# Performance work log

Hardware: AMD Instinct MI355X
Metric: run time of the kernel (lower is better)

## Reference

```python
import jax, jax.numpy as jnp
import numpy as np

B, S, E = 2, 4096, 2560
H, HKV, D = 8, 4, 256
WINDOW = 1024
SOFTCAP = 50.0
SCALING = 256.0 ** -0.5  # query_pre_attn_scalar = 256
EPS = 1e-6
MASK_VAL = -2.3819763e38


def rms_norm(x, w):
    # RMSNorm with add_unit_offset=True, computed in float32
    xf = x.astype(jnp.float32)
    out = xf * jax.lax.rsqrt(jnp.mean(xf * xf, axis=-1, keepdims=True) + EPS)
    return (out * (1.0 + w.astype(jnp.float32))).astype(x.dtype)


def apply_rotary_emb(x, cos, sin):
    # x: [B, S, h, D]; cos/sin: [S, D/2]; half-split rotation
    x1, x2 = jnp.split(x, 2, axis=-1)
    c = cos[None, :, None, :]
    s = sin[None, :, None, :]
    return jnp.concatenate([x1 * c - x2 * s, x2 * c + x1 * s], axis=-1)


def setup_inputs() -> dict:
    key = jax.random.key(0)
    ks = jax.random.split(key, 6)
    hidden_states = jax.random.normal(ks[0], (B, S, E), dtype=jnp.float32)
    # RoPE frequencies, theta=10000
    inv_freq = 1.0 / (10000.0 ** (np.arange(0, D, 2, dtype=np.float32) / D))
    t = np.arange(S, dtype=np.float32)
    freqs = np.outer(t, inv_freq)  # [S, D/2]
    freqs_cos = jnp.asarray(np.cos(freqs), dtype=jnp.float32)
    freqs_sin = jnp.asarray(np.sin(freqs), dtype=jnp.float32)
    kv_write_indices = jnp.arange(S, dtype=jnp.int32)
    k_cache = jnp.zeros((B, S, HKV, D), dtype=jnp.float32)
    v_cache = jnp.zeros((B, S, HKV, D), dtype=jnp.float32)
    # causal mask and causal+sliding-window mask (additive)
    i = np.arange(S)[:, None]
    j = np.arange(S)[None, :]
    causal = j <= i
    sliding = causal & ((i - j) < WINDOW)
    mask = jnp.asarray(np.where(causal, 0.0, MASK_VAL), dtype=jnp.float32)
    mask = jnp.broadcast_to(mask[None, None], (B, 1, S, S))
    local_mask = jnp.asarray(np.where(sliding, 0.0, MASK_VAL), dtype=jnp.float32)
    local_mask = jnp.broadcast_to(local_mask[None, None], (B, 1, S, S))
    w_qkv = jax.random.normal(ks[1], ((H + 2 * HKV) * D, E), dtype=jnp.float32) * (E ** -0.5)
    w_o = jax.random.normal(ks[2], (E, H * D), dtype=jnp.float32) * ((H * D) ** -0.5)
    q_norm_w = jnp.zeros((D,), dtype=jnp.float32)
    k_norm_w = jnp.zeros((D,), dtype=jnp.float32)
    return dict(hidden_states=hidden_states, freqs_cos=freqs_cos, freqs_sin=freqs_sin,
                kv_write_indices=kv_write_indices, k_cache=k_cache, v_cache=v_cache,
                mask=mask, local_mask=local_mask, w_qkv=w_qkv, w_o=w_o,
                q_norm_w=q_norm_w, k_norm_w=k_norm_w)


def reference(hidden_states, freqs_cos, freqs_sin, kv_write_indices, k_cache, v_cache,
              mask, local_mask, w_qkv, w_o, q_norm_w, k_norm_w):
    bsz, input_len, _ = hidden_states.shape
    qkv = jnp.einsum('bse,fe->bsf', hidden_states, w_qkv)
    xq, xk, xv = jnp.split(qkv, [H * D, H * D + HKV * D], axis=-1)
    xq = xq.reshape(bsz, input_len, H, D)
    xk = xk.reshape(bsz, input_len, HKV, D)
    xv = xv.reshape(bsz, input_len, HKV, D)
    # QK RMSNorm
    xq = rms_norm(xq, q_norm_w)
    xk = rms_norm(xk, k_norm_w)
    # RoPE
    xq = apply_rotary_emb(xq, freqs_cos, freqs_sin)
    xk = apply_rotary_emb(xk, freqs_cos, freqs_sin)
    # KV cache write
    k_cache = k_cache.at[:, kv_write_indices].set(xk)
    v_cache = v_cache.at[:, kv_write_indices].set(xv)
    kv_len = k_cache.shape[1]
    # GQA expand: [B, T, HKV, D] -> [B, T, H, D]
    nrep = H // HKV
    key = jnp.repeat(k_cache, nrep, axis=2)
    value = jnp.repeat(v_cache, nrep, axis=2)
    q = jnp.transpose(xq, (0, 2, 1, 3)) * SCALING   # [B, H, S, D]
    k = jnp.transpose(key, (0, 2, 1, 3))            # [B, H, T, D]
    v = jnp.transpose(value, (0, 2, 1, 3))
    scores = jnp.einsum('bhqd,bhkd->bhqk', q, k)
    # logit softcapping
    scores = jnp.tanh(scores / SOFTCAP) * SOFTCAP
    # attn_type == LOCAL_SLIDING -> use local (sliding-window) mask
    scores = scores + local_mask
    probs = jax.nn.softmax(scores.astype(jnp.float32), axis=-1).astype(q.dtype)
    out = jnp.einsum('bhqk,bhkd->bhqd', probs, v)
    out = jnp.transpose(out, (0, 2, 1, 3)).reshape(bsz, input_len, H * D)
    return jnp.einsum('bsf,ef->bse', out, w_o)
```

## Files before the change

### kernel.cpp

```cpp
#include <hip/hip_runtime.h>
#include <stdint.h>
#include <stddef.h>

#define B_    2
#define S_    4096
#define E_    2560
#define H_    8
#define HKV_  4
#define D_    256
#define F_    4096
#define HD_   2048
#define WIN_  1024
#define MASKNEG (-3.0e38f)

typedef __bf16 bf16;
typedef bf16  bf16x8 __attribute__((ext_vector_type(8)));
typedef bf16  bf16x4 __attribute__((ext_vector_type(4)));
typedef float f32x4  __attribute__((ext_vector_type(4)));
typedef uint32_t u32;

__device__ __forceinline__ void gl_lds16(const void* g, void* l) {
  __builtin_amdgcn_global_load_lds((const __attribute__((address_space(1))) void*)g,
                                   (__attribute__((address_space(3))) void*)l, 16, 0, 0);
}

__device__ __forceinline__ float softcap50(float x) {
  float t = x * 0.02f;
  t = fminf(fmaxf(t, -15.f), 15.f);
  float e = __expf(2.f * t);
  return 50.f * ((e - 1.f) / (e + 1.f));
}

__device__ __forceinline__ u32 pkbf16(float a, float b) {
  union { bf16 h[2]; u32 u; } cv;
  cv.h[0] = (bf16)a; cv.h[1] = (bf16)b; return cv.u;
}

__global__ __launch_bounds__(256) void to_bf16_plain(const float* __restrict__ src,
                                                     bf16* __restrict__ dst, int n) {
  const int i = (blockIdx.x * 256 + threadIdx.x) * 8;
  if (i >= n) return;
  f32x4 a = *(const f32x4*)(src + i);
  f32x4 b = *(const f32x4*)(src + i + 4);
  bf16x8 o;
#pragma unroll
  for (int j = 0; j < 4; ++j) { o[j] = (bf16)a[j]; o[j + 4] = (bf16)b[j]; }
  *(bf16x8*)(dst + i) = o;
}

__global__ __launch_bounds__(256) void gemm1_bf(const bf16* __restrict__ A,
                                                const bf16* __restrict__ W,
                                                bf16* __restrict__ qo,
                                                bf16* __restrict__ ko,
                                                bf16* __restrict__ vto,
                                                int row_base) {
  __shared__ bf16 As[128 * 32];
  __shared__ bf16 Bs[128 * 32];
  const int tid  = threadIdx.x;
  const int lane = tid & 63;
  const int l16  = lane & 15;
  const int quad = lane >> 4;
  const int wave = tid >> 6;
  const int wm   = wave & 1;
  const int wn   = wave >> 1;

  const int lrow0 = blockIdx.y * 128;
  const int col0  = blockIdx.x * 128;

  const int srow = tid >> 2;
  const int scol = (tid & 3) * 8;

  const bf16* Ab = A + (size_t)lrow0 * E_ + scol;
  const bf16* Bb = W + (size_t)col0 * E_ + scol;

  f32x4 acc[4][4] = {};

  for (int k0 = 0; k0 < E_; k0 += 32) {
    gl_lds16(Ab + (size_t)srow * E_ + k0,        As + tid * 8);
    gl_lds16(Ab + (size_t)(srow + 64) * E_ + k0, As + 2048 + tid * 8);
    gl_lds16(Bb + (size_t)srow * E_ + k0,        Bs + tid * 8);
    gl_lds16(Bb + (size_t)(srow + 64) * E_ + k0, Bs + 2048 + tid * 8);
    __syncthreads();

    bf16x8 af[4], bfr[4];
#pragma unroll
    for (int i = 0; i < 4; ++i)
      af[i] = *(const bf16x8*)&As[(wm * 64 + i * 16 + l16) * 32 + quad * 8];
#pragma unroll
    for (int i = 0; i < 4; ++i)
      bfr[i] = *(const bf16x8*)&Bs[(wn * 64 + i * 16 + l16) * 32 + quad * 8];
#pragma unroll
    for (int i = 0; i < 4; ++i)
#pragma unroll
      for (int j = 0; j < 4; ++j)
        acc[i][j] = __builtin_amdgcn_mfma_f32_16x16x32_bf16(af[i], bfr[j], acc[i][j], 0, 0, 0);
    __syncthreads();
  }

#pragma unroll
  for (int i = 0; i < 4; ++i) {
    const int rbase = row_base + lrow0 + wm * 64 + i * 16 + quad * 4;
#pragma unroll
    for (int j = 0; j < 4; ++j) {
      const int c = col0 + wn * 64 + j * 16 + l16;
      int head = c >> 8;
      const int d = c & 255;
      if (head < 12) {
        bf16* base;
        int nh;
        if (head < 8) { base = qo; nh = H_; }
        else          { base = ko; nh = HKV_; head -= 8; }
#pragma unroll
        for (int rr = 0; rr < 4; ++rr) {
          const int row = rbase + rr;
          const int b = row >> 12, s = row & 4095;
          base[(((size_t)(b * nh + head) * S_) + s) * D_ + d] = (bf16)acc[i][j][rr];
        }
      } else {
        const int kh = head - 12;
        const int b  = rbase >> 12, s0 = rbase & 4095;
        bf16x4 pk;
#pragma unroll
        for (int rr = 0; rr < 4; ++rr) pk[rr] = (bf16)acc[i][j][rr];
        *(bf16x4*)(vto + (((size_t)(b * HKV_ + kh) * D_ + d) * S_ + s0)) = pk;
      }
    }
  }
}

__global__ __launch_bounds__(192) void normrope2(
    bf16* __restrict__ q, bf16* __restrict__ k,
    const float* __restrict__ fcos, const float* __restrict__ fsin,
    const int* __restrict__ widx,
    const float* __restrict__ qnw, const float* __restrict__ knw) {
  const int bx  = blockIdx.x;
  const int b   = bx >> 12;
  const int s   = bx & 4095;
  const int tid = threadIdx.x;
  const int hh  = tid >> 4;
  const int g   = tid & 15;
  const int d0  = g * 16;

  const bool isq = (hh < 8);
  bf16* rowp = isq ? (q + (((size_t)(b * H_ + hh) * S_ + s) * D_ + d0))
                   : (k + (((size_t)(b * HKV_ + (hh - 8)) * S_ + s) * D_ + d0));
  float x[16];
  {
    bf16x8 v0 = *(const bf16x8*)rowp;
    bf16x8 v1 = *(const bf16x8*)(rowp + 8);
#pragma unroll
    for (int i = 0; i < 8; ++i) { x[i] = (float)v0[i]; x[i + 8] = (float)v1[i]; }
  }

  float ssq = 0.f;
#pragma unroll
  for (int i = 0; i < 16; ++i) ssq += x[i] * x[i];
#pragma unroll
  for (int off = 1; off < 16; off <<= 1) ssq += __shfl_xor(ssq, off);
  const float sc = rsqrtf(ssq * (1.0f / 256.0f) + 1e-6f);
  const float* w = isq ? qnw : knw;
#pragma unroll
  for (int i = 0; i < 16; ++i) x[i] = x[i] * sc * (1.0f + w[d0 + i]);

  const int fbase = (g < 8) ? d0 : (d0 - 128);
  const float* cp = fcos + (size_t)s * 128 + fbase;
  const float* sp = fsin + (size_t)s * 128 + fbase;
#pragma unroll
  for (int i = 0; i < 16; ++i) {
    const float c = cp[i], sn = sp[i];
    const float other = __shfl_xor(x[i], 8);
    x[i] = (g < 8) ? (x[i] * c - other * sn)
                   : (x[i] * c + other * sn);
  }
  if (isq) {
#pragma unroll
    for (int i = 0; i < 16; ++i) x[i] *= 0.0625f;
  }

  bf16x8 o0, o1;
#pragma unroll
  for (int i = 0; i < 8; ++i) { o0[i] = (bf16)x[i]; o1[i] = (bf16)x[i + 8]; }

  bf16* dstp = isq ? rowp
                   : (k + (((size_t)(b * HKV_ + (hh - 8)) * S_ + widx[s]) * D_ + d0));
  *(bf16x8*)dstp = o0;
  *(bf16x8*)(dstp + 8) = o1;
}

__global__ __launch_bounds__(256) void attn_mfma(const bf16* __restrict__ Q,
                                                 const bf16* __restrict__ K,
                                                 const bf16* __restrict__ Vt,
                                                 bf16* __restrict__ out) {
  __shared__ bf16 Ks[2][32 * 256];
  __shared__ bf16 Vs[2][256 * 32];

  const int hw  = blockIdx.x;
  const int lid = (hw & 7) * 128 + (hw >> 3);
  const int bx  = lid & 63;
  const int bh  = lid >> 6;
  const int b   = bh >> 3, h = bh & 7, kh = h >> 1;

  const int lane = threadIdx.x & 63;
  const int wave = threadIdx.x >> 6;
  const int l16  = lane & 15;
  const int qd   = lane >> 4;
  const int swz  = l16 & 7;

  const int q0w = bx * 64 + wave * 16;
  const int iq  = q0w + l16;

  const bf16* Kb = K  + ((size_t)(b * HKV_ + kh) * S_) * D_;
  const bf16* Vb = Vt + ((size_t)(b * HKV_ + kh) * D_) * S_;

  bf16x8 qf[8];
  {
    const bf16* qp = Q + (((size_t)(b * H_ + h) * S_ + iq) * D_) + qd * 8;
#pragma unroll
    for (int kc = 0; kc < 8; ++kc) qf[kc] = *(const bf16x8*)(qp + kc * 32);
  }

  f32x4 Od[16] = {};
  float m = MASKNEG, l = 0.f;

  int lo = bx * 64 - (WIN_ - 1); if (lo < 0) lo = 0;
  lo &= ~31;
  const int t1 = bx * 64 + 32;

  auto stage = [&](int buf, int kt) {
#pragma unroll
    for (int i = 0; i < 4; ++i) {
      const int r0  = wave * 8 + i * 2;
      const int row = r0 + (lane >> 5);
      const int c   = lane & 31;
      gl_lds16(Kb + (size_t)(kt + row) * D_ + ((c ^ (row & 7)) * 8),
               &Ks[buf][r0 * 256] + lane * 8);
    }
#pragma unroll
    for (int i = 0; i < 4; ++i) {
      const int d0 = (wave * 4 + i) * 16;
      const int d  = d0 + (lane >> 2);
      gl_lds16(Vb + (size_t)d * S_ + kt + (lane & 3) * 8,
               &Vs[buf][d0 * 32] + lane * 8);
    }
  };

  stage(0, lo);
  int buf = 0;

  for (int kt = lo; kt <= t1; kt += 32) {
    const bool pre = (kt + 32 <= t1);
    if (pre) {
      stage(buf ^ 1, kt + 32);
      asm volatile("s_waitcnt vmcnt(8)" ::: "memory");
    } else {
      asm volatile("s_waitcnt vmcnt(0)" ::: "memory");
    }
    __builtin_amdgcn_s_barrier();
    asm volatile("" ::: "memory");

    const bool dead = (kt > q0w + 15) || (kt + 31 < q0w - (WIN_ - 1));
    if (!dead) {
      f32x4 sacc[2] = {};
#pragma unroll
      for (int kc = 0; kc < 8; ++kc) {
        const int ch = ((kc * 4 + qd) ^ swz) * 8;
        bf16x8 k0 = *(const bf16x8*)&Ks[buf][l16 * 256 + ch];
        bf16x8 k1 = *(const bf16x8*)&Ks[buf][(l16 + 16) * 256 + ch];
        sacc[0] = __builtin_amdgcn_mfma_f32_16x16x32_bf16(k0, qf[kc], sacc[0], 0, 0, 0);
        sacc[1] = __builtin_amdgcn_mfma_f32_16x16x32_bf16(k1, qf[kc], sacc[1], 0, 0, 0);
      }

      float scv[8];
#pragma unroll
      for (int t = 0; t < 2; ++t)
#pragma unroll
        for (int r = 0; r < 4; ++r) {
          const int jj = kt + t * 16 + qd * 4 + r;
          const float a = softcap50(sacc[t][r]);
          scv[t * 4 + r] = (jj <= iq && (iq - jj) < WIN_) ? a : MASKNEG;
        }

      float mx = scv[0];
#pragma unroll
      for (int i = 1; i < 8; ++i) mx = fmaxf(mx, scv[i]);
      mx = fmaxf(mx, __shfl_xor(mx, 16));
      mx = fmaxf(mx, __shfl_xor(mx, 32));
      const float mn = fmaxf(m, mx);
      const float alpha = __expf(m - mn);

      float p[8], ls = 0.f;
#pragma unroll
      for (int i = 0; i < 8; ++i) {
        p[i] = (scv[i] > -1e37f) ? __expf(scv[i] - mn) : 0.f;
        ls += p[i];
      }
      ls += __shfl_xor(ls, 16);
      ls += __shfl_xor(ls, 32);
      l = l * alpha + ls;
      m = mn;
#pragma unroll
      for (int dt = 0; dt < 16; ++dt) Od[dt] *= alpha;

      const u32 w0 = pkbf16(p[0], p[1]);
      const u32 w1 = pkbf16(p[2], p[3]);
      const u32 w2 = pkbf16(p[4], p[5]);
      const u32 w3 = pkbf16(p[6], p[7]);
      const int sA = l16 + ((2 * qd) & 3) * 16;
      const int sB = l16 + ((2 * qd + 1) & 3) * 16;
      const int a0 = __shfl((int)w0, sA), a1 = __shfl((int)w1, sA);
      const int a2 = __shfl((int)w2, sA), a3 = __shfl((int)w3, sA);
      const int b0 = __shfl((int)w0, sB), b1 = __shfl((int)w1, sB);
      const int b2 = __shfl((int)w2, sB), b3 = __shfl((int)w3, sB);
      const bool thi = (qd >> 1) != 0;
      union { int i4[4]; bf16x8 v; } pf;
      pf.i4[0] = thi ? a2 : a0;
      pf.i4[1] = thi ? a3 : a1;
      pf.i4[2] = thi ? b2 : b0;
      pf.i4[3] = thi ? b3 : b1;

#pragma unroll
      for (int dt = 0; dt < 16; ++dt) {
        bf16x8 vf = *(const bf16x8*)&Vs[buf][(dt * 16 + l16) * 32 + qd * 8];
        Od[dt] = __builtin_amdgcn_mfma_f32_16x16x32_bf16(vf, pf.v, Od[dt], 0, 0, 0);
      }
    }

    asm volatile("" ::: "memory");
    __builtin_amdgcn_s_barrier();
    buf ^= 1;
  }

  const float inv = 1.f / l;
  bf16* op = out + ((size_t)b * S_ + iq) * HD_ + h * D_ + qd * 4;
#pragma unroll
  for (int dt = 0; dt < 16; ++dt) {
    bf16x4 o4;
#pragma unroll
    for (int r = 0; r < 4; ++r) o4[r] = (bf16)(Od[dt][r] * inv);
    *(bf16x4*)(op + dt * 16) = o4;
  }
}

__global__ __launch_bounds__(256) void gemm_bt_f32out(const bf16* __restrict__ A,
                                                      const bf16* __restrict__ Bw,
                                                      float* __restrict__ C,
                                                      int M, int N, int K) {
  __shared__ bf16 As[128 * 32];
  __shared__ bf16 Bs[128 * 32];
  const int tid  = threadIdx.x;
  const int lane = tid & 63;
  const int l16  = lane & 15;
  const int quad = lane >> 4;
  const int wave = tid >> 6;
  const int wm   = wave & 1;
  const int wn   = wave >> 1;

  const int row0 = blockIdx.y * 128;
  const int col0 = blockIdx.x * 128;

  const int srow = tid >> 2;
  const int scol = (tid & 3) * 8;

  const bf16* Ab = A  + (size_t)row0 * K + scol;
  const bf16* Bb = Bw + (size_t)col0 * K + scol;

  f32x4 acc[4][4] = {};

  for (int k0 = 0; k0 < K; k0 += 32) {
    gl_lds16(Ab + (size_t)srow * K + k0,        As + tid * 8);
    gl_lds16(Ab + (size_t)(srow + 64) * K + k0, As + 2048 + tid * 8);
    gl_lds16(Bb + (size_t)srow * K + k0,        Bs + tid * 8);
    gl_lds16(Bb + (size_t)(srow + 64) * K + k0, Bs + 2048 + tid * 8);
    __syncthreads();

    bf16x8 af[4], bfr[4];
#pragma unroll
    for (int i = 0; i < 4; ++i)
      af[i] = *(const bf16x8*)&As[(wm * 64 + i * 16 + l16) * 32 + quad * 8];
#pragma unroll
    for (int i = 0; i < 4; ++i)
      bfr[i] = *(const bf16x8*)&Bs[(wn * 64 + i * 16 + l16) * 32 + quad * 8];
#pragma unroll
    for (int i = 0; i < 4; ++i)
#pragma unroll
      for (int j = 0; j < 4; ++j)
        acc[i][j] = __builtin_amdgcn_mfma_f32_16x16x32_bf16(af[i], bfr[j], acc[i][j], 0, 0, 0);
    __syncthreads();
  }

#pragma unroll
  for (int i = 0; i < 4; ++i) {
    const int r = row0 + wm * 64 + i * 16 + quad * 4;
#pragma unroll
    for (int j = 0; j < 4; ++j) {
      const int c = col0 + wn * 64 + j * 16 + l16;
#pragma unroll
      for (int rr = 0; rr < 4; ++rr)
        C[(size_t)(r + rr) * N + c] = acc[i][j][rr];
    }
  }
}

extern "C" void kernel_launch(void* const* d_in, const int* in_sizes, int n_in,
                              void* d_out, int out_size, void* d_ws, size_t ws_size,
                              hipStream_t stream) {
  const float* hidden = (const float*)d_in[0];
  const float* fcos   = (const float*)d_in[1];
  const float* fsin   = (const float*)d_in[2];
  const int*   widx   = (const int*)d_in[3];
  const float* wqkv   = (const float*)d_in[8];
  const float* wo     = (const float*)d_in[9];
  const float* qnw    = (const float*)d_in[10];
  const float* knw    = (const float*)d_in[11];
  float* out = (float*)d_out;

  char* ws = (char*)d_ws;
  const size_t MB = 1024 * 1024;
  const bool big = ws_size >= 126 * MB;

  bf16* wb_bf = (bf16*)(ws);
  bf16* hb_bf = (bf16*)(ws + 20 * MB);
  bf16* q_ws  = (bf16*)(ws + (big ? 60 : 32) * MB);
  bf16* k_ws  = (bf16*)(ws + (big ? 92 : 64) * MB);
  bf16* vt_ws = (bf16*)(ws + (big ? 108 : 80) * MB);
  bf16* att_o = (bf16*)(ws);
  bf16* wo_bf = (bf16*)(ws + 32 * MB);

  to_bf16_plain<<<(F_ * E_ / 8 + 255) / 256, 256, 0, stream>>>(wqkv, wb_bf, F_ * E_);

  const int nch   = big ? 1 : 4;
  const int chrow = (B_ * S_) / nch;
  for (int c = 0; c < nch; ++c) {
    const int row_base = c * chrow;
    to_bf16_plain<<<(chrow * E_ / 8 + 255) / 256, 256, 0, stream>>>(
        hidden + (size_t)row_base * E_, hb_bf, chrow * E_);
    gemm1_bf<<<dim3(F_ / 128, chrow / 128), 256, 0, stream>>>(hb_bf, wb_bf,
                                                              q_ws, k_ws, vt_ws, row_base);
  }

  normrope2<<<dim3(B_ * S_), 192, 0, stream>>>(q_ws, k_ws, fcos, fsin, widx, qnw, knw);
  attn_mfma<<<dim3(1024), 256, 0, stream>>>(q_ws, k_ws, vt_ws, att_o);
  to_bf16_plain<<<(E_ * HD_ / 8 + 255) / 256, 256, 0, stream>>>(wo, wo_bf, E_ * HD_);
  gemm_bt_f32out<<<dim3(E_ / 128, (B_ * S_) / 128), 256, 0, stream>>>(att_o, wo_bf, out,
                                                                      B_ * S_, E_, HD_);
  (void)in_sizes; (void)n_in; (void)out_size;
}
```

Before: 892.1 us.

## Replace both GEMMs with 256x256 double-buffered eight-phase pipelined MFMA kernel

Both projection GEMMs now use one templated kernel with 256x256 output tiles, 512 threads and a K step of 64. LDS holds two buffers, and global-to-LDS loads for the next stages are interleaved with MFMA phases separated by barriers and raised s_setprio. The LDS layout uses an XOR swizzle to avoid bank conflicts, and block ids are remapped for L2 locality. The aim is to hide memory latency behind compute and raise arithmetic intensity per tile. The cost is 128KB of LDS per block and many more accumulator registers, which limits occupancy.

```diff
diff --git a/kernel.cpp b/kernel.cpp
--- a/kernel.cpp
+++ b/kernel.cpp
@@ -24,6 +24,12 @@
                                    (__attribute__((address_space(3))) void*)l, 16, 0, 0);
 }
 
+__device__ __forceinline__ void bar_mf() {
+  asm volatile("" ::: "memory");
+  __builtin_amdgcn_s_barrier();
+  asm volatile("" ::: "memory");
+}
+
 __device__ __forceinline__ float softcap50(float x) {
   float t = x * 0.02f;
   t = fminf(fmaxf(t, -15.f), 15.f);
@@ -48,81 +54,155 @@
   *(bf16x8*)(dst + i) = o;
 }
 
-__global__ __launch_bounds__(256) void gemm1_bf(const bf16* __restrict__ A,
-                                                const bf16* __restrict__ W,
-                                                bf16* __restrict__ qo,
-                                                bf16* __restrict__ ko,
-                                                bf16* __restrict__ vto,
-                                                int row_base) {
-  __shared__ bf16 As[128 * 32];
-  __shared__ bf16 Bs[128 * 32];
+template <int EPI>
+__global__ __launch_bounds__(512, 2) void gemm_8ph(
+    const bf16* __restrict__ A, const bf16* __restrict__ Bw, int Kd, int NT,
+    bf16* __restrict__ qo, bf16* __restrict__ ko, bf16* __restrict__ vto,
+    float* __restrict__ C, int Nout, int row_base) {
+  __shared__ bf16 Lds[2][4][128 * 64];
+
   const int tid  = threadIdx.x;
   const int lane = tid & 63;
+  const int wave = tid >> 6;
+  const int wm   = wave >> 2;
+  const int wn   = wave & 3;
   const int l16  = lane & 15;
   const int quad = lane >> 4;
-  const int wave = tid >> 6;
-  const int wm   = wave & 1;
-  const int wn   = wave >> 1;
-
-  const int lrow0 = blockIdx.y * 128;
-  const int col0  = blockIdx.x * 128;
-
-  const int srow = tid >> 2;
-  const int scol = (tid & 3) * 8;
-
-  const bf16* Ab = A + (size_t)lrow0 * E_ + scol;
-  const bf16* Bb = W + (size_t)col0 * E_ + scol;
-
-  f32x4 acc[4][4] = {};
-
-  for (int k0 = 0; k0 < E_; k0 += 32) {
-    gl_lds16(Ab + (size_t)srow * E_ + k0,        As + tid * 8);
-    gl_lds16(Ab + (size_t)(srow + 64) * E_ + k0, As + 2048 + tid * 8);
-    gl_lds16(Bb + (size_t)srow * E_ + k0,        Bs + tid * 8);
-    gl_lds16(Bb + (size_t)(srow + 64) * E_ + k0, Bs + 2048 + tid * 8);
-    __syncthreads();
-
-    bf16x8 af[4], bfr[4];
-#pragma unroll
-    for (int i = 0; i < 4; ++i)
-      af[i] = *(const bf16x8*)&As[(wm * 64 + i * 16 + l16) * 32 + quad * 8];
-#pragma unroll
-    for (int i = 0; i < 4; ++i)
-      bfr[i] = *(const bf16x8*)&Bs[(wn * 64 + i * 16 + l16) * 32 + quad * 8];
-#pragma unroll
-    for (int i = 0; i < 4; ++i)
-#pragma unroll
-      for (int j = 0; j < 4; ++j)
-        acc[i][j] = __builtin_amdgcn_mfma_f32_16x16x32_bf16(af[i], bfr[j], acc[i][j], 0, 0, 0);
-    __syncthreads();
-  }
-
-#pragma unroll
-  for (int i = 0; i < 4; ++i) {
-    const int rbase = row_base + lrow0 + wm * 64 + i * 16 + quad * 4;
+
+  const int nwg  = gridDim.x * gridDim.y;
+  const int obid = blockIdx.y * gridDim.x + blockIdx.x;
+  const int bid  = (obid & 7) * (nwg >> 3) + (obid >> 3);
+  const int mt   = bid / gridDim.x;
+  const int ntl  = bid - mt * gridDim.x;
+  const int row0 = mt * 256, col0 = ntl * 256;
+
+  const bf16* Ah[2] = {A  + (size_t)row0 * Kd, A  + (size_t)(row0 + 128) * Kd};
+  const bf16* Bh[2] = {Bw + (size_t)col0 * Kd, Bw + (size_t)(col0 + 128) * Kd};
+
+  auto stage = [&](int dbf, int hf, const bf16* src, int k0) {
+#pragma unroll
+    for (int i = 0; i < 2; ++i) {
+      const int g = tid + i * 512;
+      const int r = g >> 3, c = g & 7;
+      gl_lds16(src + (size_t)r * Kd + k0 + ((c ^ (r & 7)) << 3),
+               &Lds[dbf][hf][0] + g * 8);
+    }
+  };
+  auto rdA = [&](int dbf, int i, int ks) -> bf16x8 {
+    const int r = i * 16 + l16;
+    return *(const bf16x8*)&Lds[dbf][wm][r * 64 + (((ks * 4 + quad) ^ (r & 7)) << 3)];
+  };
+  auto rdB = [&](int dbf, int j, int ks) -> bf16x8 {
+    const int r = (wn & 1) * 64 + j * 16 + l16;
+    return *(const bf16x8*)&Lds[dbf][2 + (wn >> 1)][r * 64 + (((ks * 4 + quad) ^ (r & 7)) << 3)];
+  };
+
+  f32x4 acc[8][4] = {};
+
+  stage(0, 0, Ah[0], 0); stage(0, 1, Ah[1], 0);
+  stage(0, 2, Bh[0], 0); stage(0, 3, Bh[1], 0);
+  if (NT > 1) { stage(1, 2, Bh[0], 64); stage(1, 3, Bh[1], 64); }
+  asm volatile("s_waitcnt vmcnt(4)" ::: "memory");
+  bar_mf();
+
+  int db = 0;
+  for (int t = 0; t < NT; ++t, db ^= 1) {
+    const int k1 = (t + 1) * 64, k2 = (t + 2) * 64;
+    const bool st1 = (t + 1 < NT), st2 = (t + 2 < NT);
+
+    bf16x8 bfr[4][2], a[4][2], a2[4][2];
+#pragma unroll
+    for (int j = 0; j < 4; ++j) { bfr[j][0] = rdB(db, j, 0); bfr[j][1] = rdB(db, j, 1); }
+#pragma unroll
+    for (int i = 0; i < 4; ++i) { a[i][0] = rdA(db, i, 0); a[i][1] = rdA(db, i, 1); }
+    if (st1) stage(db ^ 1, 0, Ah[0], k1);
+    bar_mf();
+    __builtin_amdgcn_s_setprio(1);
+#pragma unroll
+    for (int i = 0; i < 2; ++i)
+#pragma unroll
+      for (int j = 0; j < 4; ++j) {
+        acc[i][j] = __builtin_amdgcn_mfma_f32_16x16x32_bf16(a[i][0], bfr[j][0], acc[i][j], 0, 0, 0);
+        acc[i][j] = __builtin_amdgcn_mfma_f32_16x16x32_bf16(a[i][1], bfr[j][1], acc[i][j], 0, 0, 0);
+      }
+    __builtin_amdgcn_s_setprio(0);
+    bar_mf();
+
+#pragma unroll
+    for (int i = 0; i < 4; ++i) { a2[i][0] = rdA(db, i + 4, 0); a2[i][1] = rdA(db, i + 4, 1); }
+    if (st1) stage(db ^ 1, 1, Ah[1], k1);
+    bar_mf();
+    __builtin_amdgcn_s_setprio(1);
+#pragma unroll
+    for (int i = 2; i < 4; ++i)
+#pragma unroll
+      for (int j = 0; j < 4; ++j) {
+        acc[i][j] = __builtin_amdgcn_mfma_f32_16x16x32_bf16(a[i][0], bfr[j][0], acc[i][j], 0, 0, 0);
+        acc[i][j] = __builtin_amdgcn_mfma_f32_16x16x32_bf16(a[i][1], bfr[j][1], acc[i][j], 0, 0, 0);
+      }
+    __builtin_amdgcn_s_setprio(0);
+    bar_mf();
+
+    if (st2) stage(db, 2, Bh[0], k2);
+    bar_mf();
+    __builtin_amdgcn_s_setprio(1);
+#pragma unroll
+    for (int i = 0; i < 2; ++i)
+#pragma unroll
+      for (int j = 0; j < 4; ++j) {
+        acc[i + 4][j] = __builtin_amdgcn_mfma_f32_16x16x32_bf16(a2[i][0], bfr[j][0], acc[i + 4][j], 0, 0, 0);
+        acc[i + 4][j] = __builtin_amdgcn_mfma_f32_16x16x32_bf16(a2[i][1], bfr[j][1], acc[i + 4][j], 0, 0, 0);
+      }
+    __builtin_amdgcn_s_setprio(0);
+    bar_mf();
+
+    if (st2) stage(db, 3, Bh[1], k2);
+    bar_mf();
+    __builtin_amdgcn_s_setprio(1);
+#pragma unroll
+    for (int i = 2; i < 4; ++i)
+#pragma unroll
+      for (int j = 0; j < 4; ++j) {
+        acc[i + 4][j] = __builtin_amdgcn_mfma_f32_16x16x32_bf16(a2[i][0], bfr[j][0], acc[i + 4][j], 0, 0, 0);
+        acc[i + 4][j] = __builtin_amdgcn_mfma_f32_16x16x32_bf16(a2[i][1], bfr[j][1], acc[i + 4][j], 0, 0, 0);
+      }
+    __builtin_amdgcn_s_setprio(0);
+    if (st2) asm volatile("s_waitcnt vmcnt(4)" ::: "memory");
+    else     asm volatile("s_waitcnt vmcnt(0)" ::: "memory");
+    bar_mf();
+  }
+
+#pragma unroll
+  for (int i = 0; i < 8; ++i) {
+    const int rbase = row_base + row0 + wm * 128 + i * 16 + quad * 4;
 #pragma unroll
     for (int j = 0; j < 4; ++j) {
       const int c = col0 + wn * 64 + j * 16 + l16;
-      int head = c >> 8;
-      const int d = c & 255;
-      if (head < 12) {
-        bf16* base;
-        int nh;
-        if (head < 8) { base = qo; nh = H_; }
-        else          { base = ko; nh = HKV_; head -= 8; }
-#pragma unroll
-        for (int rr = 0; rr < 4; ++rr) {
-          const int row = rbase + rr;
-          const int b = row >> 12, s = row & 4095;
-          base[(((size_t)(b * nh + head) * S_) + s) * D_ + d] = (bf16)acc[i][j][rr];
+      if constexpr (EPI == 1) {
+        int head = c >> 8;
+        const int d = c & 255;
+        if (head < 12) {
+          bf16* base; int nh;
+          if (head < 8) { base = qo; nh = H_; }
+          else          { base = ko; nh = HKV_; head -= 8; }
+#pragma unroll
+          for (int rr = 0; rr < 4; ++rr) {
+            const int row = rbase + rr;
+            const int bb = row >> 12, s = row & 4095;
+            base[(((size_t)(bb * nh + head) * S_) + s) * D_ + d] = (bf16)acc[i][j][rr];
+          }
+        } else {
+          const int kh = head - 12;
+          const int bb = rbase >> 12, s0 = rbase & 4095;
+          bf16x4 pk;
+#pragma unroll
+          for (int rr = 0; rr < 4; ++rr) pk[rr] = (bf16)acc[i][j][rr];
+          *(bf16x4*)(vto + (((size_t)(bb * HKV_ + kh) * D_ + d) * S_ + s0)) = pk;
         }
       } else {
-        const int kh = head - 12;
-        const int b  = rbase >> 12, s0 = rbase & 4095;
-        bf16x4 pk;
-#pragma unroll
-        for (int rr = 0; rr < 4; ++rr) pk[rr] = (bf16)acc[i][j][rr];
-        *(bf16x4*)(vto + (((size_t)(b * HKV_ + kh) * D_ + d) * S_ + s0)) = pk;
+#pragma unroll
+        for (int rr = 0; rr < 4; ++rr)
+          C[(size_t)(rbase + rr) * Nout + c] = acc[i][j][rr];
       }
     }
   }
@@ -341,66 +421,6 @@
   }
 }
 
-__global__ __launch_bounds__(256) void gemm_bt_f32out(const bf16* __restrict__ A,
-                                                      const bf16* __restrict__ Bw,
-                                                      float* __restrict__ C,
-                                                      int M, int N, int K) {
-  __shared__ bf16 As[128 * 32];
-  __shared__ bf16 Bs[128 * 32];
-  const int tid  = threadIdx.x;
-  const int lane = tid & 63;
-  const int l16  = lane & 15;
-  const int quad = lane >> 4;
-  const int wave = tid >> 6;
-  const int wm   = wave & 1;
-  const int wn   = wave >> 1;
-
-  const int row0 = blockIdx.y * 128;
-  const int col0 = blockIdx.x * 128;
-
-  const int srow = tid >> 2;
-  const int scol = (tid & 3) * 8;
-
-  const bf16* Ab = A  + (size_t)row0 * K + scol;
-  const bf16* Bb = Bw + (size_t)col0 * K + scol;
-
-  f32x4 acc[4][4] = {};
-
-  for (int k0 = 0; k0 < K; k0 += 32) {
-    gl_lds16(Ab + (size_t)srow * K + k0,        As + tid * 8);
-    gl_lds16(Ab + (size_t)(srow + 64) * K + k0, As + 2048 + tid * 8);
-    gl_lds16(Bb + (size_t)srow * K + k0,        Bs + tid * 8);
-    gl_lds16(Bb + (size_t)(srow + 64) * K + k0, Bs + 2048 + tid * 8);
-    __syncthreads();
-
-    bf16x8 af[4], bfr[4];
-#pragma unroll
-    for (int i = 0; i < 4; ++i)
-      af[i] = *(const bf16x8*)&As[(wm * 64 + i * 16 + l16) * 32 + quad * 8];
-#pragma unroll
-    for (int i = 0; i < 4; ++i)
-      bfr[i] = *(const bf16x8*)&Bs[(wn * 64 + i * 16 + l16) * 32 + quad * 8];
-#pragma unroll
-    for (int i = 0; i < 4; ++i)
-#pragma unroll
-      for (int j = 0; j < 4; ++j)
-        acc[i][j] = __builtin_amdgcn_mfma_f32_16x16x32_bf16(af[i], bfr[j], acc[i][j], 0, 0, 0);
-    __syncthreads();
-  }
-
-#pragma unroll
-  for (int i = 0; i < 4; ++i) {
-    const int r = row0 + wm * 64 + i * 16 + quad * 4;
-#pragma unroll
-    for (int j = 0; j < 4; ++j) {
-      const int c = col0 + wn * 64 + j * 16 + l16;
-#pragma unroll
-      for (int rr = 0; rr < 4; ++rr)
-        C[(size_t)(r + rr) * N + c] = acc[i][j][rr];
-    }
-  }
-}
-
 extern "C" void kernel_launch(void* const* d_in, const int* in_sizes, int n_in,
                               void* d_out, int out_size, void* d_ws, size_t ws_size,
                               hipStream_t stream) {
@@ -434,14 +454,14 @@
     const int row_base = c * chrow;
     to_bf16_plain<<<(chrow * E_ / 8 + 255) / 256, 256, 0, stream>>>(
         hidden + (size_t)row_base * E_, hb_bf, chrow * E_);
-    gemm1_bf<<<dim3(F_ / 128, chrow / 128), 256, 0, stream>>>(hb_bf, wb_bf,
-                                                              q_ws, k_ws, vt_ws, row_base);
+    gemm_8ph<1><<<dim3(F_ / 256, chrow / 256), 512, 0, stream>>>(
+        hb_bf, wb_bf, E_, E_ / 64, q_ws, k_ws, vt_ws, nullptr, 0, row_base);
   }
 
   normrope2<<<dim3(B_ * S_), 192, 0, stream>>>(q_ws, k_ws, fcos, fsin, widx, qnw, knw);
   attn_mfma<<<dim3(1024), 256, 0, stream>>>(q_ws, k_ws, vt_ws, att_o);
   to_bf16_plain<<<(E_ * HD_ / 8 + 255) / 256, 256, 0, stream>>>(wo, wo_bf, E_ * HD_);
-  gemm_bt_f32out<<<dim3(E_ / 128, (B_ * S_) / 128), 256, 0, stream>>>(att_o, wo_bf, out,
-                                                                      B_ * S_, E_, HD_);
+  gemm_8ph<0><<<dim3(E_ / 256, (B_ * S_) / 256), 512, 0, stream>>>(
+      att_o, wo_bf, HD_, HD_ / 64, nullptr, nullptr, nullptr, out, E_, 0);
   (void)in_sizes; (void)n_in; (void)out_size;
 }
```

After: 858.3 us. 3.8% less time.
